# Optimization experiments

Measured on AMD Instinct MI355X. Metric: run time of the kernel, lower is better.

Reference implementation:

```python
import jax, jax.numpy as jnp
import numpy as np

E = 1024   # d_model
H = 16     # nhead
DH = E // H
F = 4096   # dim_feedforward
B, S = 4, 1024
EPS = 1e-5


def setup_inputs() -> dict:
    key = jax.random.key(0)
    ks = jax.random.split(key, 12)
    s = 0.02
    return {
        "src": jax.random.normal(ks[0], (B, S, E), jnp.float32),
        "src_mask": jnp.zeros((S, S), jnp.float32),
        "w_qkv": jax.random.normal(ks[1], (3 * E, E), jnp.float32) * s,
        "b_qkv": jnp.zeros((3 * E,), jnp.float32),
        "w_o": jax.random.normal(ks[2], (E, E), jnp.float32) * s,
        "b_o": jnp.zeros((E,), jnp.float32),
        "w1": jax.random.normal(ks[3], (F, E), jnp.float32) * s,
        "b1": jnp.zeros((F,), jnp.float32),
        "w2": jax.random.normal(ks[4], (E, F), jnp.float32) * s,
        "b2": jnp.zeros((E,), jnp.float32),
        "ln1_g": jnp.ones((E,), jnp.float32),
        "ln1_b": jnp.zeros((E,), jnp.float32),
        "ln2_g": jnp.ones((E,), jnp.float32),
        "ln2_b": jnp.zeros((E,), jnp.float32),
    }


def _layer_norm(x, g, b):
    mu = jnp.mean(x, axis=-1, keepdims=True)
    var = jnp.mean(jnp.square(x - mu), axis=-1, keepdims=True)
    return (x - mu) * jax.lax.rsqrt(var + EPS) * g + b


def reference(src, src_mask, w_qkv, b_qkv, w_o, b_o, w1, b1, w2, b2,
              ln1_g, ln1_b, ln2_g, ln2_b):
    # dropout in eval mode (identity). Math matches nn.MultiheadAttention
    # with need_weights=True, average_attn_weights=False.
    b, s, e = src.shape
    qkv = src @ w_qkv.T + b_qkv                      # [B,S,3E]
    q, k, v = jnp.split(qkv, 3, axis=-1)
    q = q.reshape(b, s, H, DH)
    k = k.reshape(b, s, H, DH)
    v = v.reshape(b, s, H, DH)
    scale = 1.0 / np.sqrt(DH)
    scores = jnp.einsum('bqhd,bkhd->bhqk', q, k) * scale + src_mask  # [B,H,S,S]
    attn_weights = jax.nn.softmax(scores, axis=-1)                   # [B,H,S,S]
    ctx = jnp.einsum('bhqk,bkhd->bqhd', attn_weights, v).reshape(b, s, e)
    attn_out = ctx @ w_o.T + b_o
    x = _layer_norm(src + attn_out, ln1_g, ln1_b)
    ffn = jax.nn.relu(x @ w1.T + b1) @ w2.T + b2
    x = _layer_norm(x + ffn, ln2_g, ln2_b)
    return x, attn_weights
```

## Files before the change

kernel.cpp:

```cpp
#include <hip/hip_runtime.h>
#include <cstdint>

typedef __bf16 bf16;
typedef bf16 bf16x8 __attribute__((ext_vector_type(8)));
typedef bf16 bf16x4 __attribute__((ext_vector_type(4)));
typedef float f32x4 __attribute__((ext_vector_type(4)));
typedef uint32_t u32;

static constexpr int E_ = 1024;
static constexpr int H_ = 16;
static constexpr int DH_ = 64;
static constexpr int F_ = 4096;
static constexpr int B_ = 4;
static constexpr int S_ = 1024;
static constexpr long TOK = (long)B_ * S_;

__device__ static __forceinline__ void gld16(const void* g, void* l) {
  __builtin_amdgcn_global_load_lds(
      (const __attribute__((address_space(1))) u32*)g,
      (__attribute__((address_space(3))) u32*)l, 16, 0, 0);
}

__device__ __forceinline__ f32x4 mfma16(bf16x8 a, bf16x8 b, f32x4 c) {
  return __builtin_amdgcn_mfma_f32_16x16x32_bf16(a, b, c, 0, 0, 0);
}

__global__ __launch_bounds__(256) void f2b_all(
    const float* __restrict__ s0, bf16* __restrict__ d0,
    const float* __restrict__ s1, bf16* __restrict__ d1,
    const float* __restrict__ s2, bf16* __restrict__ d2,
    const float* __restrict__ s3, bf16* __restrict__ d3,
    const float* __restrict__ s4, bf16* __restrict__ d4) {
  long v = (long)blockIdx.x * 256 + threadIdx.x;
  const float* in;
  bf16* out;
  long off;
  if (v < 524288)        { in = s0; out = d0; off = v; }
  else if (v < 917504)   { in = s1; out = d1; off = v - 524288; }
  else if (v < 1048576)  { in = s2; out = d2; off = v - 917504; }
  else if (v < 1572864)  { in = s3; out = d3; off = v - 1048576; }
  else                   { in = s4; out = d4; off = v - 1572864; }
  const float4* p = (const float4*)in + off * 2;
  float4 a = p[0], b = p[1];
  bf16x8 o = {(bf16)a.x, (bf16)a.y, (bf16)a.z, (bf16)a.w,
              (bf16)b.x, (bf16)b.y, (bf16)b.z, (bf16)b.w};
  *((bf16x8*)out + off) = o;
}

enum { G_RELU_BF16 = 0, G_QKV = 1 };

template <int EPI>
__global__ __launch_bounds__(512, 2) void gemm256(
    const bf16* __restrict__ A, const bf16* __restrict__ Bm,
    bf16* __restrict__ Cb, bf16* __restrict__ Qh, bf16* __restrict__ Kh,
    bf16* __restrict__ Vt, const float* __restrict__ bias, int K, int ldc) {
  __shared__ bf16 S[65536];
  bf16* A0 = S;
  bf16* A1 = S + 16384;
  bf16* B0 = S + 32768;
  bf16* B1 = S + 49152;
  const int tid = threadIdx.x, lane = tid & 63, wave = tid >> 6;
  const int quad = lane >> 4, l16 = lane & 15;
  const int wm = wave >> 2, wn = wave & 3;
  const int sx = ((l16 >> 2) & 1) << 4;
  const int row0 = blockIdx.y * 256, col0 = blockIdx.x * 256;
  const int NT = K >> 6;

  const long ldab = (long)K * 2;
  const int cbs = ((tid & 7) * 16) ^ (((tid >> 5) & 1) << 5);
  const char* Ag = (const char*)A + (long)(row0 + (tid >> 3)) * ldab + cbs;
  const char* Bg = (const char*)Bm + (long)(col0 + (tid >> 3)) * ldab + cbs;
  char* A0c = (char*)A0 + tid * 16;
  char* A1c = (char*)A1 + tid * 16;
  char* B0c = (char*)B0 + tid * 16;
  char* B1c = (char*)B1 + tid * 16;

  f32x4 acc[8][4];
#pragma unroll
  for (int m = 0; m < 8; m++)
#pragma unroll
    for (int n = 0; n < 4; n++) acc[m][n] = (f32x4){0.f, 0.f, 0.f, 0.f};

#pragma unroll
  for (int c = 0; c < 4; c++) gld16(Ag + (long)c * 64 * ldab, A0c + c * 8192);
#pragma unroll
  for (int c = 0; c < 4; c++) gld16(Bg + (long)c * 64 * ldab, B0c + c * 8192);
#pragma unroll
  for (int c = 0; c < 4; c++) gld16(Ag + (long)c * 64 * ldab + 128, A1c + c * 8192);

  auto tile = [&](int kt, const bf16* Ac, const bf16* Bc, char* AcS, char* BoS,
                  bool last) {
    if (last)
      asm volatile("s_waitcnt vmcnt(0)" ::: "memory");
    else
      asm volatile("s_waitcnt vmcnt(4)" ::: "memory");
    __builtin_amdgcn_sched_barrier(0);
    __builtin_amdgcn_s_barrier();
    __builtin_amdgcn_sched_barrier(0);
    bf16x8 af[4][2], bfr[4][2];
    if (kt + 1 < NT) {
      gld16(Bg + (long)(kt + 1) * 128, BoS);
      gld16(Bg + (long)64 * ldab + (long)(kt + 1) * 128, BoS + 8192);
    }
#pragma unroll
    for (int mi = 0; mi < 4; mi++)
#pragma unroll
      for (int kk = 0; kk < 2; kk++)
        af[mi][kk] = *(const bf16x8*)&Ac[(wm * 128 + mi * 16 + l16) * 64 +
                                         ((kk * 32 + quad * 8) ^ sx)];
#pragma unroll
    for (int n = 0; n < 4; n++) {
#pragma unroll
      for (int kk = 0; kk < 2; kk++)
        bfr[n][kk] = *(const bf16x8*)&Bc[(wn * 64 + n * 16 + l16) * 64 +
                                         ((kk * 32 + quad * 8) ^ sx)];
      __builtin_amdgcn_s_setprio(1);
#pragma unroll
      for (int mi = 0; mi < 4; mi++)
#pragma unroll
        for (int kk = 0; kk < 2; kk++)
          acc[mi][n] = mfma16(af[mi][kk], bfr[n][kk], acc[mi][n]);
      __builtin_amdgcn_s_setprio(0);
    }
    if (kt + 1 < NT) {
      gld16(Bg + (long)2 * 64 * ldab + (long)(kt + 1) * 128, BoS + 16384);
      gld16(Bg + (long)3 * 64 * ldab + (long)(kt + 1) * 128, BoS + 24576);
    }
#pragma unroll
    for (int mi = 0; mi < 4; mi++)
#pragma unroll
      for (int kk = 0; kk < 2; kk++)
        af[mi][kk] = *(const bf16x8*)&Ac[(wm * 128 + 64 + mi * 16 + l16) * 64 +
                                         ((kk * 32 + quad * 8) ^ sx)];
    asm volatile("s_waitcnt lgkmcnt(0)" ::: "memory");
    __builtin_amdgcn_sched_barrier(0);
    __builtin_amdgcn_s_barrier();
    __builtin_amdgcn_sched_barrier(0);
#pragma unroll
    for (int n = 0; n < 4; n++) {
      if (n == 1 && kt + 2 < NT) {
        gld16(Ag + (long)(kt + 2) * 128, AcS);
        gld16(Ag + (long)64 * ldab + (long)(kt + 2) * 128, AcS + 8192);
      }
      if (n == 2 && kt + 2 < NT) {
        gld16(Ag + (long)2 * 64 * ldab + (long)(kt + 2) * 128, AcS + 16384);
        gld16(Ag + (long)3 * 64 * ldab + (long)(kt + 2) * 128, AcS + 24576);
      }
      __builtin_amdgcn_s_setprio(1);
#pragma unroll
      for (int mi = 0; mi < 4; mi++)
#pragma unroll
        for (int kk = 0; kk < 2; kk++)
          acc[4 + mi][n] = mfma16(af[mi][kk], bfr[n][kk], acc[4 + mi][n]);
      __builtin_amdgcn_s_setprio(0);
    }
  };

  for (int kt = 0; kt < NT; kt += 2) {
    tile(kt, A0, B0, A0c, B1c, false);
    tile(kt + 1, A1, B1, A1c, B0c, kt + 2 == NT);
  }

  if constexpr (EPI == G_RELU_BF16) {
#pragma unroll
    for (int m = 0; m < 8; m++)
#pragma unroll
      for (int n = 0; n < 4; n++)
#pragma unroll
        for (int r = 0; r < 4; r++) {
          int row = row0 + wm * 128 + m * 16 + quad * 4 + r;
          int col = col0 + wn * 64 + n * 16 + l16;
          float v = acc[m][n][r] + bias[col];
          Cb[(long)row * ldc + col] = (bf16)fmaxf(v, 0.f);
        }
  } else {
    const int which = col0 >> 10;
    if (which == 2) {
      asm volatile("s_waitcnt lgkmcnt(0) vmcnt(0)" ::: "memory");
      __builtin_amdgcn_s_barrier();
      bf16* T = S;
#pragma unroll
      for (int m = 0; m < 8; m++)
#pragma unroll
        for (int n = 0; n < 4; n++)
#pragma unroll
          for (int r = 0; r < 4; r++) {
            int row_l = wm * 128 + m * 16 + quad * 4 + r;
            int col_l = wn * 64 + n * 16 + l16;
            float t = acc[m][n][r] + bias[col0 + col_l];
            T[col_l * 256 + (row_l ^ ((col_l & 7) << 4))] = (bf16)t;
          }
      __syncthreads();
      const int b_ = row0 >> 10;
      const int s0 = row0 & 1023;
#pragma unroll
      for (int g = 0; g < 8; g++) {
        int col_l = wave * 32 + g * 4 + quad;
        int nn = (col0 + col_l) & 1023;
        int h_ = nn >> 6, d_ = nn & 63;
#pragma unroll
        for (int half = 0; half < 2; half++) {
          int sl = l16 * 8 + half * 128;
          bf16x8 vv = *(const bf16x8*)&T[col_l * 256 + (sl ^ ((col_l & 7) << 4))];
          *(bf16x8*)&Vt[(((long)(b_ * H_ + h_)) * DH_ + d_) * S_ + s0 + sl] = vv;
        }
      }
    } else {
#pragma unroll
      for (int m = 0; m < 8; m++)
#pragma unroll
        for (int n = 0; n < 4; n++)
#pragma unroll
          for (int r = 0; r < 4; r++) {
            int row = row0 + wm * 128 + m * 16 + quad * 4 + r;
            int col = col0 + wn * 64 + n * 16 + l16;
            float t = acc[m][n][r] + bias[col];
            int b_ = row >> 10, s_ = row & 1023;
            int nn = col & 1023;
            int h_ = nn >> 6, d_ = nn & 63;
            long q = (((long)(b_ * H_ + h_)) * S_ + s_) * DH_ + d_;
            if (which == 0) Qh[q] = (bf16)t;
            else Kh[q] = (bf16)t;
          }
    }
  }
}

enum { EPI_BIAS_RES_F32 = 3 };

template <int EPI, int BN>
__global__ __launch_bounds__(256, 2) void gemm_nt(
    const bf16* __restrict__ A, const bf16* __restrict__ Bm,
    float* __restrict__ Cf, bf16* __restrict__ Cb,
    const float* __restrict__ bias, const float* __restrict__ res,
    int K, int ldc) {
  constexpr int NJ = BN / 32;
  __shared__ bf16 Sm[128 * 64 + BN * 64];
  bf16* As = Sm;
  bf16* Bs = Sm + 128 * 64;
  const int tid = threadIdx.x, lane = tid & 63, wave = tid >> 6;
  const int quad = lane >> 4, l16 = lane & 15;
  const int wm = wave >> 1, wn = wave & 1;
  const int row0 = blockIdx.y * 128, col0 = blockIdx.x * BN;

  const long ldab = (long)K * 2;
  const char* Ag = (const char*)A +
                   (long)(row0 + wave * 32 + (lane >> 3)) * ldab + (lane & 7) * 16;
  const char* Bg = (const char*)Bm +
                   (long)(col0 + wave * (BN / 4) + (lane >> 3)) * ldab + (lane & 7) * 16;
  char* Al = (char*)As + (wave * 32 + (lane >> 3)) * 128 + (lane & 7) * 16;
  char* Bl = (char*)Bs + (wave * (BN / 4) + (lane >> 3)) * 128 + (lane & 7) * 16;

  f32x4 acc[4][NJ];
#pragma unroll
  for (int i = 0; i < 4; i++)
#pragma unroll
    for (int j = 0; j < NJ; j++) acc[i][j] = (f32x4){0.f, 0.f, 0.f, 0.f};

  for (int k0 = 0; k0 < K; k0 += 64) {
    __syncthreads();
#pragma unroll
    for (int c = 0; c < 4; c++) gld16(Ag + (long)c * 8 * ldab + k0 * 2, Al + c * 1024);
#pragma unroll
    for (int c = 0; c < BN / 32; c++) gld16(Bg + (long)c * 8 * ldab + k0 * 2, Bl + c * 1024);
    __syncthreads();
#pragma unroll
    for (int kk = 0; kk < 2; kk++) {
      bf16x8 af[4], bfr[NJ];
#pragma unroll
      for (int i = 0; i < 4; i++)
        af[i] = *(const bf16x8*)&As[(wm * 64 + i * 16 + l16) * 64 + kk * 32 + quad * 8];
#pragma unroll
      for (int j = 0; j < NJ; j++)
        bfr[j] = *(const bf16x8*)&Bs[(wn * (BN / 2) + j * 16 + l16) * 64 + kk * 32 + quad * 8];
#pragma unroll
      for (int i = 0; i < 4; i++)
#pragma unroll
        for (int j = 0; j < NJ; j++) acc[i][j] = mfma16(af[i], bfr[j], acc[i][j]);
    }
  }

#pragma unroll
  for (int i = 0; i < 4; i++)
#pragma unroll
    for (int j = 0; j < NJ; j++)
#pragma unroll
      for (int r = 0; r < 4; r++) {
        int row = row0 + wm * 64 + i * 16 + quad * 4 + r;
        int col = col0 + wn * (BN / 2) + j * 16 + l16;
        float v = acc[i][j][r];
        if constexpr (EPI == EPI_BIAS_RES_F32) {
          Cf[(long)row * ldc + col] = v + bias[col] + res[(long)row * ldc + col];
        } else {
          Cb[(long)row * ldc + col] = (bf16)fmaxf(v + bias[col], 0.f);
        }
      }
}

__global__ __launch_bounds__(256, 2) void attn_pass1(
    const bf16* __restrict__ Q, const bf16* __restrict__ K,
    const float* __restrict__ mask, float* __restrict__ rowsum) {
  __shared__ bf16 Qs[128 * 64];
  __shared__ bf16 Ks[128 * 64];
  const int tid = threadIdx.x, lane = tid & 63, wave = tid >> 6;
  const int quad = lane >> 4, l16 = lane & 15;
  const int q0 = blockIdx.x * 128, bh = blockIdx.y;
  const bf16* Qb = Q + ((long)bh * S_ + q0) * DH_;
  const bf16* Kb = K + (long)bh * S_ * DH_;

  {
    const char* g = (const char*)Qb + wave * 4096 + lane * 16;
    char* l = (char*)Qs + wave * 4096 + lane * 16;
#pragma unroll
    for (int c = 0; c < 4; c++) gld16(g + c * 1024, l + c * 1024);
  }

  float rs[2][4];
#pragma unroll
  for (int i = 0; i < 2; i++)
#pragma unroll
    for (int r = 0; r < 4; r++) rs[i][r] = 0.f;

  for (int t = 0; t < 8; t++) {
    __syncthreads();
    {
      const char* g = (const char*)Kb + (long)t * 16384 + wave * 4096 + lane * 16;
      char* l = (char*)Ks + wave * 4096 + lane * 16;
#pragma unroll
      for (int c = 0; c < 4; c++) gld16(g + c * 1024, l + c * 1024);
    }
    __syncthreads();
    f32x4 acc[2][8];
#pragma unroll
    for (int i = 0; i < 2; i++)
#pragma unroll
      for (int j = 0; j < 8; j++) acc[i][j] = (f32x4){0.f, 0.f, 0.f, 0.f};
#pragma unroll
    for (int kk = 0; kk < 2; kk++) {
      bf16x8 af[2], bfr[8];
#pragma unroll
      for (int i = 0; i < 2; i++)
        af[i] = *(const bf16x8*)&Qs[(wave * 32 + i * 16 + l16) * 64 + kk * 32 + quad * 8];
#pragma unroll
      for (int j = 0; j < 8; j++)
        bfr[j] = *(const bf16x8*)&Ks[(j * 16 + l16) * 64 + kk * 32 + quad * 8];
#pragma unroll
      for (int i = 0; i < 2; i++)
#pragma unroll
        for (int j = 0; j < 8; j++) acc[i][j] = mfma16(af[i], bfr[j], acc[i][j]);
    }
#pragma unroll
    for (int i = 0; i < 2; i++)
#pragma unroll
      for (int j = 0; j < 8; j++)
#pragma unroll
        for (int r = 0; r < 4; r++) {
          int qr = q0 + wave * 32 + i * 16 + quad * 4 + r;
          int gcol = t * 128 + j * 16 + l16;
          float sv = acc[i][j][r] * 0.125f + mask[(long)qr * S_ + gcol];
          rs[i][r] += __expf(sv);
        }
  }
#pragma unroll
  for (int i = 0; i < 2; i++)
#pragma unroll
    for (int r = 0; r < 4; r++) {
      float v = rs[i][r];
      v += __shfl_xor(v, 1);
      v += __shfl_xor(v, 2);
      v += __shfl_xor(v, 4);
      v += __shfl_xor(v, 8);
      if (l16 == 0)
        rowsum[(long)bh * S_ + q0 + wave * 32 + i * 16 + quad * 4 + r] = v;
    }
}

__global__ __launch_bounds__(256, 2) void attn_pass2(
    const bf16* __restrict__ Q, const bf16* __restrict__ K,
    const bf16* __restrict__ V, const float* __restrict__ mask,
    const float* __restrict__ rowsum, float* __restrict__ W,
    bf16* __restrict__ ctxb) {
  __shared__ bf16 Qs[128 * 64];
  __shared__ bf16 Ks[128 * 64];
  __shared__ bf16 Ps[128 * 136];
  const int tid = threadIdx.x, lane = tid & 63, wave = tid >> 6;
  const int quad = lane >> 4, l16 = lane & 15;
  const int q0 = blockIdx.x * 128, bh = blockIdx.y;
  const bf16* Qb = Q + ((long)bh * S_ + q0) * DH_;
  const bf16* Kb = K + (long)bh * S_ * DH_;
  const bf16* Vb = V + (long)bh * DH_ * S_;

  float rinv[2][4];
#pragma unroll
  for (int i = 0; i < 2; i++)
#pragma unroll
    for (int r = 0; r < 4; r++)
      rinv[i][r] =
          1.0f / rowsum[(long)bh * S_ + q0 + wave * 32 + i * 16 + quad * 4 + r];

  {
    const char* g = (const char*)Qb + wave * 4096 + lane * 16;
    char* l = (char*)Qs + wave * 4096 + lane * 16;
#pragma unroll
    for (int c = 0; c < 4; c++) gld16(g + c * 1024, l + c * 1024);
  }

  f32x4 cacc[2][4];
#pragma unroll
  for (int i = 0; i < 2; i++)
#pragma unroll
    for (int j = 0; j < 4; j++) cacc[i][j] = (f32x4){0.f, 0.f, 0.f, 0.f};

  for (int t = 0; t < 8; t++) {
    __syncthreads();
    {
      const char* g = (const char*)Kb + (long)t * 16384 + wave * 4096 + lane * 16;
      char* l = (char*)Ks + wave * 4096 + lane * 16;
#pragma unroll
      for (int c = 0; c < 4; c++) gld16(g + c * 1024, l + c * 1024);
    }
    __syncthreads();
    f32x4 acc[2][8];
#pragma unroll
    for (int i = 0; i < 2; i++)
#pragma unroll
      for (int j = 0; j < 8; j++) acc[i][j] = (f32x4){0.f, 0.f, 0.f, 0.f};
#pragma unroll
    for (int kk = 0; kk < 2; kk++) {
      bf16x8 af[2], bfr[8];
#pragma unroll
      for (int i = 0; i < 2; i++)
        af[i] = *(const bf16x8*)&Qs[(wave * 32 + i * 16 + l16) * 64 + kk * 32 + quad * 8];
#pragma unroll
      for (int j = 0; j < 8; j++)
        bfr[j] = *(const bf16x8*)&Ks[(j * 16 + l16) * 64 + kk * 32 + quad * 8];
#pragma unroll
      for (int i = 0; i < 2; i++)
#pragma unroll
        for (int j = 0; j < 8; j++) acc[i][j] = mfma16(af[i], bfr[j], acc[i][j]);
    }
#pragma unroll
    for (int i = 0; i < 2; i++)
#pragma unroll
      for (int j = 0; j < 8; j++)
#pragma unroll
        for (int r = 0; r < 4; r++) {
          int ql = wave * 32 + i * 16 + quad * 4 + r;
          int qr = q0 + ql;
          int col = j * 16 + l16, gcol = t * 128 + col;
          float u = __expf(acc[i][j][r] * 0.125f + mask[(long)qr * S_ + gcol]) *
                    rinv[i][r];
          __builtin_nontemporal_store(u, &W[((long)bh * S_ + qr) * S_ + gcol]);
          Ps[ql * 136 + col] = (bf16)u;
        }
    __syncthreads();
#pragma unroll
    for (int kk = 0; kk < 4; kk++) {
      bf16x8 pf[2], vf[4];
#pragma unroll
      for (int i = 0; i < 2; i++)
        pf[i] = *(const bf16x8*)&Ps[(wave * 32 + i * 16 + l16) * 136 + kk * 32 + quad * 8];
#pragma unroll
      for (int j = 0; j < 4; j++)
        vf[j] = *(const bf16x8*)(Vb + (long)(j * 16 + l16) * S_ + t * 128 +
                                 kk * 32 + quad * 8);
#pragma unroll
      for (int i = 0; i < 2; i++)
#pragma unroll
        for (int j = 0; j < 4; j++) cacc[i][j] = mfma16(pf[i], vf[j], cacc[i][j]);
    }
  }
  const int b_ = bh >> 4, h_ = bh & 15;
#pragma unroll
  for (int i = 0; i < 2; i++)
#pragma unroll
    for (int j = 0; j < 4; j++)
#pragma unroll
      for (int r = 0; r < 4; r++) {
        int qr = q0 + wave * 32 + i * 16 + quad * 4 + r;
        ctxb[((long)b_ * S_ + qr) * E_ + h_ * 64 + j * 16 + l16] =
            (bf16)cacc[i][j][r];
      }
}

__global__ __launch_bounds__(256) void ln_kernel(
    const float* __restrict__ a, const float* __restrict__ g,
    const float* __restrict__ beta, float* __restrict__ outf,
    bf16* __restrict__ outb) {
  const int tid = threadIdx.x;
  const int wave = tid >> 6, lane = tid & 63;
  long base = (long)blockIdx.x * E_ + tid * 4;
  float4 x = *(const float4*)(a + base);
  float s = x.x + x.y + x.z + x.w;
  float sq = x.x * x.x + x.y * x.y + x.z * x.z + x.w * x.w;
#pragma unroll
  for (int o = 32; o; o >>= 1) { s += __shfl_xor(s, o); sq += __shfl_xor(sq, o); }
  __shared__ float rs[4], rq[4];
  if (!lane) { rs[wave] = s; rq[wave] = sq; }
  __syncthreads();
  s = rs[0] + rs[1] + rs[2] + rs[3];
  sq = rq[0] + rq[1] + rq[2] + rq[3];
  float mu = s * (1.f / E_);
  float var = sq * (1.f / E_) - mu * mu;
  float rstd = rsqrtf(var + 1e-5f);
  int c = tid * 4;
  float4 gg = *(const float4*)(g + c);
  float4 bb = *(const float4*)(beta + c);
  float o0 = (x.x - mu) * rstd * gg.x + bb.x;
  float o1 = (x.y - mu) * rstd * gg.y + bb.y;
  float o2 = (x.z - mu) * rstd * gg.z + bb.z;
  float o3 = (x.w - mu) * rstd * gg.w + bb.w;
  if (outf) *(float4*)(outf + base) = make_float4(o0, o1, o2, o3);
  if (outb) {
    bf16x4 ob = {(bf16)o0, (bf16)o1, (bf16)o2, (bf16)o3};
    *(bf16x4*)(outb + base) = ob;
  }
}

extern "C" void kernel_launch(void* const* d_in, const int* in_sizes, int n_in,
                              void* d_out, int out_size, void* d_ws, size_t ws_size,
                              hipStream_t stream) {
  const float* src   = (const float*)d_in[0];
  const float* mask  = (const float*)d_in[1];
  const float* w_qkv = (const float*)d_in[2];
  const float* b_qkv = (const float*)d_in[3];
  const float* w_o   = (const float*)d_in[4];
  const float* b_o   = (const float*)d_in[5];
  const float* w1    = (const float*)d_in[6];
  const float* b1    = (const float*)d_in[7];
  const float* w2    = (const float*)d_in[8];
  const float* b2    = (const float*)d_in[9];
  const float* ln1g  = (const float*)d_in[10];
  const float* ln1b  = (const float*)d_in[11];
  const float* ln2g  = (const float*)d_in[12];
  const float* ln2b  = (const float*)d_in[13];

  float* out = (float*)d_out;
  float* attnW = out + TOK * E_;

  char* w = (char*)d_ws;
  auto alloc = [&](size_t bytes) {
    void* p = w;
    w += (bytes + 255) & ~(size_t)255;
    return p;
  };
  bf16* srcb  = (bf16*)alloc(TOK * E_ * 2);
  bf16* wqkvb = (bf16*)alloc((size_t)3 * E_ * E_ * 2);
  bf16* wob   = (bf16*)alloc((size_t)E_ * E_ * 2);
  bf16* w1b   = (bf16*)alloc((size_t)F_ * E_ * 2);
  bf16* w2b   = (bf16*)alloc((size_t)E_ * F_ * 2);
  bf16* Qh    = (bf16*)alloc((size_t)B_ * H_ * S_ * DH_ * 2);
  bf16* Kh    = (bf16*)alloc((size_t)B_ * H_ * S_ * DH_ * 2);
  bf16* Vt    = (bf16*)alloc((size_t)B_ * H_ * DH_ * S_ * 2);
  bf16* ctxb  = (bf16*)alloc(TOK * E_ * 2);
  float* attn_out = (float*)alloc(TOK * E_ * 4);
  float* x1f  = (float*)alloc(TOK * E_ * 4);
  bf16* x1b   = (bf16*)alloc(TOK * E_ * 2);
  bf16* h1b   = (bf16*)alloc(TOK * (size_t)F_ * 2);
  float* ffn2 = (float*)alloc(TOK * E_ * 4);
  float* rowsum = (float*)alloc((size_t)B_ * H_ * S_ * 4);

  f2b_all<<<8192, 256, 0, stream>>>(src, srcb, w_qkv, wqkvb, w_o, wob,
                                    w1, w1b, w2, w2b);

  gemm256<G_QKV><<<dim3(3 * E_ / 256, TOK / 256), 512, 0, stream>>>(
      srcb, wqkvb, nullptr, Qh, Kh, Vt, b_qkv, E_, 0);

  attn_pass1<<<dim3(S_ / 128, B_ * H_), 256, 0, stream>>>(Qh, Kh, mask, rowsum);
  attn_pass2<<<dim3(S_ / 128, B_ * H_), 256, 0, stream>>>(Qh, Kh, Vt, mask,
                                                          rowsum, attnW, ctxb);

  gemm_nt<EPI_BIAS_RES_F32, 64><<<dim3(E_ / 64, TOK / 128), 256, 0, stream>>>(
      ctxb, wob, attn_out, nullptr, b_o, src, E_, E_);

  ln_kernel<<<TOK, 256, 0, stream>>>(attn_out, ln1g, ln1b, x1f, x1b);

  gemm256<G_RELU_BF16><<<dim3(F_ / 256, TOK / 256), 512, 0, stream>>>(
      x1b, w1b, h1b, nullptr, nullptr, nullptr, b1, E_, F_);

  gemm_nt<EPI_BIAS_RES_F32, 64><<<dim3(E_ / 64, TOK / 128), 256, 0, stream>>>(
      h1b, w2b, ffn2, nullptr, b2, x1f, F_, E_);

  ln_kernel<<<TOK, 256, 0, stream>>>(ffn2, ln2g, ln2b, out, nullptr);
}
```

Before: 600.5 us.

## Replace gemm_nt with double-buffered swizzled gemm128p and widen gemm256 LDS swizzle

Replaces the single-buffered 128x64 output GEMM, used for the attention output projection and FFN2, with a double-buffered pipelined kernel. It prefetches the next A and B tiles with async global-to-LDS loads, waits on explicit vmcnt/lgkmcnt and barriers, raises wave priority around the MFMAs, and XOR-swizzles the LDS layout to cut bank conflicts. The gemm256 swizzle also changes from a 1-bit to a 3-bit XOR pattern. The cost is more LDS and more complex hand-written synchronization, which could introduce ordering hazards.

```diff
diff --git a/kernel.cpp b/kernel.cpp
--- a/kernel.cpp
+++ b/kernel.cpp
@@ -62,12 +62,12 @@
   const int tid = threadIdx.x, lane = tid & 63, wave = tid >> 6;
   const int quad = lane >> 4, l16 = lane & 15;
   const int wm = wave >> 2, wn = wave & 3;
-  const int sx = ((l16 >> 2) & 1) << 4;
+  const int sx = (l16 & 7) << 3;
   const int row0 = blockIdx.y * 256, col0 = blockIdx.x * 256;
   const int NT = K >> 6;
 
   const long ldab = (long)K * 2;
-  const int cbs = ((tid & 7) * 16) ^ (((tid >> 5) & 1) << 5);
+  const int cbs = (((tid & 7) ^ ((tid >> 3) & 7))) * 16;
   const char* Ag = (const char*)A + (long)(row0 + (tid >> 3)) * ldab + cbs;
   const char* Bg = (const char*)Bm + (long)(col0 + (tid >> 3)) * ldab + cbs;
   char* A0c = (char*)A0 + tid * 16;
@@ -226,74 +226,105 @@
   }
 }
 
-enum { EPI_BIAS_RES_F32 = 3 };
-
-template <int EPI, int BN>
-__global__ __launch_bounds__(256, 2) void gemm_nt(
+__global__ __launch_bounds__(256, 2) void gemm128p(
     const bf16* __restrict__ A, const bf16* __restrict__ Bm,
-    float* __restrict__ Cf, bf16* __restrict__ Cb,
-    const float* __restrict__ bias, const float* __restrict__ res,
-    int K, int ldc) {
-  constexpr int NJ = BN / 32;
-  __shared__ bf16 Sm[128 * 64 + BN * 64];
-  bf16* As = Sm;
-  bf16* Bs = Sm + 128 * 64;
+    float* __restrict__ Cf, const float* __restrict__ bias,
+    const float* __restrict__ res, int K, int ldc) {
+  __shared__ bf16 S[24576];
+  bf16* A0 = S;
+  bf16* A1 = S + 8192;
+  bf16* B0 = S + 16384;
+  bf16* B1 = S + 20480;
   const int tid = threadIdx.x, lane = tid & 63, wave = tid >> 6;
   const int quad = lane >> 4, l16 = lane & 15;
   const int wm = wave >> 1, wn = wave & 1;
-  const int row0 = blockIdx.y * 128, col0 = blockIdx.x * BN;
+  const int sx = (l16 & 7) << 3;
+  const int row0 = blockIdx.y * 128, col0 = blockIdx.x * 64;
+  const int NT = K >> 6;
 
   const long ldab = (long)K * 2;
-  const char* Ag = (const char*)A +
-                   (long)(row0 + wave * 32 + (lane >> 3)) * ldab + (lane & 7) * 16;
-  const char* Bg = (const char*)Bm +
-                   (long)(col0 + wave * (BN / 4) + (lane >> 3)) * ldab + (lane & 7) * 16;
-  char* Al = (char*)As + (wave * 32 + (lane >> 3)) * 128 + (lane & 7) * 16;
-  char* Bl = (char*)Bs + (wave * (BN / 4) + (lane >> 3)) * 128 + (lane & 7) * 16;
-
-  f32x4 acc[4][NJ];
-#pragma unroll
-  for (int i = 0; i < 4; i++)
-#pragma unroll
-    for (int j = 0; j < NJ; j++) acc[i][j] = (f32x4){0.f, 0.f, 0.f, 0.f};
-
-  for (int k0 = 0; k0 < K; k0 += 64) {
-    __syncthreads();
-#pragma unroll
-    for (int c = 0; c < 4; c++) gld16(Ag + (long)c * 8 * ldab + k0 * 2, Al + c * 1024);
-#pragma unroll
-    for (int c = 0; c < BN / 32; c++) gld16(Bg + (long)c * 8 * ldab + k0 * 2, Bl + c * 1024);
-    __syncthreads();
-#pragma unroll
-    for (int kk = 0; kk < 2; kk++) {
-      bf16x8 af[4], bfr[NJ];
-#pragma unroll
-      for (int i = 0; i < 4; i++)
-        af[i] = *(const bf16x8*)&As[(wm * 64 + i * 16 + l16) * 64 + kk * 32 + quad * 8];
-#pragma unroll
-      for (int j = 0; j < NJ; j++)
-        bfr[j] = *(const bf16x8*)&Bs[(wn * (BN / 2) + j * 16 + l16) * 64 + kk * 32 + quad * 8];
-#pragma unroll
-      for (int i = 0; i < 4; i++)
-#pragma unroll
-        for (int j = 0; j < NJ; j++) acc[i][j] = mfma16(af[i], bfr[j], acc[i][j]);
-    }
-  }
-
-#pragma unroll
-  for (int i = 0; i < 4; i++)
-#pragma unroll
-    for (int j = 0; j < NJ; j++)
+  const int cbs = (((tid & 7) ^ ((tid >> 3) & 7))) * 16;
+  const char* Ag = (const char*)A + (long)(row0 + (tid >> 3)) * ldab + cbs;
+  const char* Bg = (const char*)Bm + (long)(col0 + (tid >> 3)) * ldab + cbs;
+  char* A0c = (char*)A0 + tid * 16;
+  char* A1c = (char*)A1 + tid * 16;
+  char* B0c = (char*)B0 + tid * 16;
+  char* B1c = (char*)B1 + tid * 16;
+
+  f32x4 acc[4][2];
+#pragma unroll
+  for (int m = 0; m < 4; m++)
+#pragma unroll
+    for (int n = 0; n < 2; n++) acc[m][n] = (f32x4){0.f, 0.f, 0.f, 0.f};
+
+#pragma unroll
+  for (int c = 0; c < 4; c++) gld16(Ag + (long)c * 32 * ldab, A0c + c * 4096);
+#pragma unroll
+  for (int c = 0; c < 2; c++) gld16(Bg + (long)c * 32 * ldab, B0c + c * 4096);
+#pragma unroll
+  for (int c = 0; c < 4; c++) gld16(Ag + (long)c * 32 * ldab + 128, A1c + c * 4096);
+
+  auto tile = [&](int kt, const bf16* Ac, const bf16* Bc, char* AcS, char* BoS,
+                  bool last) {
+    if (last)
+      asm volatile("s_waitcnt vmcnt(0)" ::: "memory");
+    else
+      asm volatile("s_waitcnt vmcnt(4)" ::: "memory");
+    __builtin_amdgcn_sched_barrier(0);
+    __builtin_amdgcn_s_barrier();
+    __builtin_amdgcn_sched_barrier(0);
+    if (kt + 1 < NT) {
+      gld16(Bg + (long)(kt + 1) * 128, BoS);
+      gld16(Bg + (long)32 * ldab + (long)(kt + 1) * 128, BoS + 4096);
+    }
+    bf16x8 af[4][2], bfr[2][2];
+#pragma unroll
+    for (int mi = 0; mi < 4; mi++)
+#pragma unroll
+      for (int kk = 0; kk < 2; kk++)
+        af[mi][kk] = *(const bf16x8*)&Ac[(wm * 64 + mi * 16 + l16) * 64 +
+                                         ((kk * 32 + quad * 8) ^ sx)];
+#pragma unroll
+    for (int nj = 0; nj < 2; nj++)
+#pragma unroll
+      for (int kk = 0; kk < 2; kk++)
+        bfr[nj][kk] = *(const bf16x8*)&Bc[(wn * 32 + nj * 16 + l16) * 64 +
+                                          ((kk * 32 + quad * 8) ^ sx)];
+    asm volatile("s_waitcnt lgkmcnt(0)" ::: "memory");
+    __builtin_amdgcn_sched_barrier(0);
+    __builtin_amdgcn_s_barrier();
+    __builtin_amdgcn_sched_barrier(0);
+    if (kt + 2 < NT) {
+#pragma unroll
+      for (int c = 0; c < 4; c++)
+        gld16(Ag + (long)c * 32 * ldab + (long)(kt + 2) * 128, AcS + c * 4096);
+    }
+    __builtin_amdgcn_s_setprio(1);
+#pragma unroll
+    for (int mi = 0; mi < 4; mi++)
+#pragma unroll
+      for (int nj = 0; nj < 2; nj++)
+#pragma unroll
+        for (int kk = 0; kk < 2; kk++)
+          acc[mi][nj] = mfma16(af[mi][kk], bfr[nj][kk], acc[mi][nj]);
+    __builtin_amdgcn_s_setprio(0);
+  };
+
+  for (int kt = 0; kt < NT; kt += 2) {
+    tile(kt, A0, B0, A0c, B1c, false);
+    tile(kt + 1, A1, B1, A1c, B0c, kt + 2 == NT);
+  }
+
+#pragma unroll
+  for (int mi = 0; mi < 4; mi++)
+#pragma unroll
+    for (int nj = 0; nj < 2; nj++)
 #pragma unroll
       for (int r = 0; r < 4; r++) {
-        int row = row0 + wm * 64 + i * 16 + quad * 4 + r;
-        int col = col0 + wn * (BN / 2) + j * 16 + l16;
-        float v = acc[i][j][r];
-        if constexpr (EPI == EPI_BIAS_RES_F32) {
-          Cf[(long)row * ldc + col] = v + bias[col] + res[(long)row * ldc + col];
-        } else {
-          Cb[(long)row * ldc + col] = (bf16)fmaxf(v + bias[col], 0.f);
-        }
+        int row = row0 + wm * 64 + mi * 16 + quad * 4 + r;
+        int col = col0 + wn * 32 + nj * 16 + l16;
+        Cf[(long)row * ldc + col] =
+            acc[mi][nj][r] + bias[col] + res[(long)row * ldc + col];
       }
 }
 
@@ -570,16 +601,16 @@
   attn_pass2<<<dim3(S_ / 128, B_ * H_), 256, 0, stream>>>(Qh, Kh, Vt, mask,
                                                           rowsum, attnW, ctxb);
 
-  gemm_nt<EPI_BIAS_RES_F32, 64><<<dim3(E_ / 64, TOK / 128), 256, 0, stream>>>(
-      ctxb, wob, attn_out, nullptr, b_o, src, E_, E_);
+  gemm128p<<<dim3(E_ / 64, TOK / 128), 256, 0, stream>>>(
+      ctxb, wob, attn_out, b_o, src, E_, E_);
 
   ln_kernel<<<TOK, 256, 0, stream>>>(attn_out, ln1g, ln1b, x1f, x1b);
 
   gemm256<G_RELU_BF16><<<dim3(F_ / 256, TOK / 256), 512, 0, stream>>>(
       x1b, w1b, h1b, nullptr, nullptr, nullptr, b1, E_, F_);
 
-  gemm_nt<EPI_BIAS_RES_F32, 64><<<dim3(E_ / 64, TOK / 128), 256, 0, stream>>>(
-      h1b, w2b, ffn2, nullptr, b2, x1f, F_, E_);
+  gemm128p<<<dim3(E_ / 64, TOK / 128), 256, 0, stream>>>(
+      h1b, w2b, ffn2, b2, x1f, F_, E_);
 
   ln_kernel<<<TOK, 256, 0, stream>>>(ffn2, ln2g, ln2b, out, nullptr);
 }
```

Result: faster. 564.4 us (-6.0%).
